# Kernel tuning notes

Hardware: AMD Instinct MI355X
Metric: run time of the kernel (lower is better)

## Reference

```python
import jax, jax.numpy as jnp
import numpy as np

E, K, D_IN, D_H, D_OUT, B = 16, 2, 256, 512, 256, 32768


def setup_inputs() -> dict:
    key = jax.random.key(0)
    ks = jax.random.split(key, 7)
    s_in = 1.0 / np.sqrt(D_IN)
    s_h = 1.0 / np.sqrt(D_H)
    return {
        "x": jax.random.normal(ks[0], (B, D_IN), jnp.float32),
        "Wg": jax.random.normal(ks[1], (D_IN, E), jnp.float32) * s_in,
        "bg": jnp.zeros((E,), jnp.float32),
        "W1": jax.random.normal(ks[2], (E, D_IN, D_H), jnp.float32) * s_in,
        "b1": jnp.zeros((E, D_H), jnp.float32),
        "W2": jax.random.normal(ks[3], (E, D_H, D_OUT), jnp.float32) * s_h,
        "b2": jnp.zeros((E, D_OUT), jnp.float32),
    }


def reference(x, Wg, bg, W1, b1, W2, b2):
    # Gating: softmax over experts, top-k, renormalize routing weights.
    probs = jax.nn.softmax(x @ Wg + bg, axis=-1)            # [B, E]
    top_vals, top_idx = jax.lax.top_k(probs, K)              # [B, K]
    w = top_vals / jnp.sum(top_vals, axis=-1, keepdims=True)  # [B, K]

    # Dense per-expert MLP over all tokens (vectorized dispatch equivalent).
    h = jax.nn.relu(jnp.einsum("bi,eih->ebh", x, W1) + b1[:, None, :])  # [E, B, Dh]
    out_e = jnp.einsum("ebh,eho->ebo", h, W2) + b2[:, None, :]          # [E, B, Do]

    # Gather each token's k assigned expert outputs and combine weighted.
    out_be = jnp.transpose(out_e, (1, 0, 2))                  # [B, E, Do]
    sel = jnp.take_along_axis(out_be, top_idx[:, :, None], axis=1)  # [B, K, Do]
    return jnp.sum(w[:, :, None] * sel, axis=1)               # [B, Do]
```

## Files before the change

### kernel.cpp

```cpp
#include <hip/hip_runtime.h>

#define E_ 16
#define DIN 256
#define DH 512
#define DOUT 256
#define BTOK 32768

typedef _Float16 half8 __attribute__((ext_vector_type(8)));
typedef _Float16 half4v __attribute__((ext_vector_type(4)));
typedef float float4v __attribute__((ext_vector_type(4)));

#define OFF_P1      0u
#define OFF_P2      4194304u
#define OFF_XH      8388608u
#define OFF_SCR     25165824u
#define OFF_TIDX    58720256u
#define OFF_TW      58982400u
#define OFF_STOK    59244544u
#define OFF_SW      59506688u
#define OFF_CNT     59768832u
#define OFF_OFFS    59768960u
#define OFF_CUR     59769088u
#define OFF_TMAP    59769216u
#define MLP_GRID    2048

__global__ __launch_bounds__(256) void pack_kernel(const float* __restrict__ W1,
                                                   const float* __restrict__ W2,
                                                   _Float16* __restrict__ p1,
                                                   _Float16* __restrict__ p2,
                                                   int* __restrict__ counts) {
    int tid = threadIdx.x;
    int bid = blockIdx.x * 4 + (tid >> 6);
    int l = tid & 63;
    int quad = l >> 4, l15 = l & 15;
    if (blockIdx.x == 0 && tid < 16) counts[tid] = 0;
    if (bid < 4096) {
        int ht = bid & 31, kt = (bid >> 5) & 7, e = bid >> 8;
        half8 v;
#pragma unroll
        for (int j = 0; j < 8; ++j)
            v[j] = (_Float16)W1[(e * DIN + kt * 32 + quad * 8 + j) * DH + ht * 16 + l15];
        ((half8*)p1)[bid * 64 + l] = v;
    } else {
        int b2i = bid - 4096;
        int ot = b2i & 15, kt = (b2i >> 4) & 15, e = b2i >> 8;
        half8 v;
#pragma unroll
        for (int j = 0; j < 8; ++j)
            v[j] = (_Float16)W2[(e * DH + kt * 32 + quad * 8 + j) * DOUT + ot * 16 + l15];
        ((half8*)p2)[b2i * 64 + l] = v;
    }
}

__global__ __launch_bounds__(256) void gate_kernel(const float* __restrict__ x,
                                                   const float* __restrict__ Wg,
                                                   const float* __restrict__ bg,
                                                   _Float16* __restrict__ xh,
                                                   int* __restrict__ tidx,
                                                   float* __restrict__ tw,
                                                   int* __restrict__ counts) {
    __shared__ float WgS[DIN * E_];
    __shared__ int hcnt[16];
    int tid = threadIdx.x;
    if (tid < 16) hcnt[tid] = 0;
#pragma unroll
    for (int i = 0; i < 4; ++i)
        ((float4v*)WgS)[tid + i * 256] = ((const float4v*)Wg)[tid + i * 256];
    __syncthreads();

    int q = tid & 7, tg = tid >> 3;
    int t0 = blockIdx.x * 64 + tg * 2;

    float acc[2][16];
#pragma unroll
    for (int tt = 0; tt < 2; ++tt)
#pragma unroll
        for (int e = 0; e < 16; ++e) acc[tt][e] = 0.f;

#pragma unroll
    for (int ii = 0; ii < 8; ++ii) {
        int kb = q * 32 + ii * 4;
        float4v xv[2];
#pragma unroll
        for (int tt = 0; tt < 2; ++tt) {
            xv[tt] = *(const float4v*)&x[(t0 + tt) * DIN + kb];
            half4v hv;
#pragma unroll
            for (int j = 0; j < 4; ++j) hv[j] = (_Float16)xv[tt][j];
            *(half4v*)&xh[(t0 + tt) * DIN + kb] = hv;
        }
#pragma unroll
        for (int j = 0; j < 4; ++j) {
            const float4v* wrow = (const float4v*)&WgS[(kb + j) * 16];
            float4v w0 = wrow[0], w1 = wrow[1], w2 = wrow[2], w3 = wrow[3];
#pragma unroll
            for (int tt = 0; tt < 2; ++tt) {
                float xs = xv[tt][j];
#pragma unroll
                for (int c = 0; c < 4; ++c) {
                    acc[tt][0 + c]  += xs * w0[c];
                    acc[tt][4 + c]  += xs * w1[c];
                    acc[tt][8 + c]  += xs * w2[c];
                    acc[tt][12 + c] += xs * w3[c];
                }
            }
        }
    }
#pragma unroll
    for (int tt = 0; tt < 2; ++tt)
#pragma unroll
        for (int e = 0; e < 16; ++e) {
            acc[tt][e] += __shfl_xor(acc[tt][e], 1);
            acc[tt][e] += __shfl_xor(acc[tt][e], 2);
            acc[tt][e] += __shfl_xor(acc[tt][e], 4);
        }
    if (q == 0) {
#pragma unroll
        for (int tt = 0; tt < 2; ++tt) {
            int b = t0 + tt;
            float m1 = -3.4e38f, m2 = -3.4e38f;
            int i1 = 0, i2 = 0;
#pragma unroll
            for (int e = 0; e < 16; ++e) {
                float v = acc[tt][e] + bg[e];
                if (v > m1) { m2 = m1; i2 = i1; m1 = v; i1 = e; }
                else if (v > m2) { m2 = v; i2 = e; }
            }
            float e2 = __expf(m2 - m1);
            float w1 = 1.f / (1.f + e2);
            tidx[b * 2] = i1; tidx[b * 2 + 1] = i2;
            tw[b * 2] = w1;  tw[b * 2 + 1] = e2 * w1;
            atomicAdd(&hcnt[i1], 1);
            atomicAdd(&hcnt[i2], 1);
        }
    }
    __syncthreads();
    if (tid < 16) atomicAdd(&counts[tid], hcnt[tid]);
}

__global__ void scan_kernel(const int* __restrict__ counts, int* __restrict__ offsets,
                            int* __restrict__ cursor, int* __restrict__ tmap) {
    __shared__ int s_off[17];
    int tid = threadIdx.x;
    for (int i = tid; i < MLP_GRID; i += 64) tmap[i] = -1;
    if (tid == 0) {
        int run = 0;
        for (int e = 0; e < 16; ++e) { s_off[e] = run; run += counts[e]; }
        s_off[16] = run;
    }
    __syncthreads();
    if (tid < 16) {
        int e = tid;
        offsets[e] = s_off[e];
        cursor[e] = s_off[e];
        if (e == 0) offsets[16] = s_off[16];
        int nt = (s_off[e + 1] - s_off[e] + 63) >> 6;
        int xc = e & 7;
        int base = (e >= 8) ? ((s_off[e - 7] - s_off[e - 8] + 63) >> 6) : 0;
        for (int t = 0; t < nt; ++t) {
            int s = base + t;
            if (s < 256) tmap[xc + 8 * s] = (e << 16) | t;
        }
    }
}

__global__ __launch_bounds__(256) void scatter_kernel(const int* __restrict__ tidx,
                                                      const float* __restrict__ tw,
                                                      int* __restrict__ cursor,
                                                      int* __restrict__ stok,
                                                      float* __restrict__ sw) {
    __shared__ int lc[16];
    __shared__ int lbase[16];
    int tid = threadIdx.x;
    if (tid < 16) lc[tid] = 0;
    __syncthreads();
    int g = blockIdx.x * 256 + tid;
    int e = tidx[g];
    int rank = atomicAdd(&lc[e], 1);
    __syncthreads();
    if (tid < 16) lbase[tid] = atomicAdd(&cursor[tid], lc[tid]);
    __syncthreads();
    int pos = lbase[e] + rank;
    stok[pos] = g;
    sw[pos] = tw[g];
}

#define XS 0
#define HS 16384
__global__ __launch_bounds__(512, 4) void mlp_kernel(const _Float16* __restrict__ xh,
                                                     const _Float16* __restrict__ p1,
                                                     const _Float16* __restrict__ p2,
                                                     const float* __restrict__ b1,
                                                     const float* __restrict__ b2,
                                                     const int* __restrict__ offsets,
                                                     const int* __restrict__ stok,
                                                     const float* __restrict__ sw,
                                                     const int* __restrict__ tmap,
                                                     _Float16* __restrict__ scr) {
    __shared__ _Float16 S[32768];
    const int tile = tmap[blockIdx.x];
    if (tile < 0) return;
    const int e = tile >> 16;
    const int ts = (tile & 0xffff) * 64;
    const int off = offsets[e];
    const int ne = offsets[e + 1] - off;
    const int rows = min(64, ne - ts);

    const int tid = threadIdx.x;
    const int w = tid >> 6;
    const int l = tid & 63;
    const int l15 = l & 15;
    const int quad = l >> 4;

#pragma unroll
    for (int j = 0; j < 4; ++j) {
        int tokl = w * 8 + j * 2 + (l >> 5);
        int slot = l & 31;
        int g = slot ^ (tokl & 7);
        int r = tokl; if (r >= rows) r = rows - 1;
        int tok = stok[off + ts + r] >> 1;
        half8 v = *(const half8*)&xh[tok * DIN + g * 8];
        *(half8*)&S[XS + tokl * 256 + slot * 8] = v;
    }

    const half8* p1b = (const half8*)p1;
    const half8* p2b = (const half8*)p2;

    float4v acc2[4][2];
#pragma unroll
    for (int mt = 0; mt < 4; ++mt)
#pragma unroll
        for (int n = 0; n < 2; ++n) acc2[mt][n] = (float4v){0.f, 0.f, 0.f, 0.f};

    __syncthreads();

#pragma unroll
    for (int half = 0; half < 2; ++half) {
        float4v acc1[2][4];
#pragma unroll
        for (int mh = 0; mh < 2; ++mh)
#pragma unroll
            for (int nt = 0; nt < 4; ++nt) acc1[mh][nt] = (float4v){0.f, 0.f, 0.f, 0.f};

#pragma unroll
        for (int kt = 0; kt < 8; ++kt) {
            half8 bq[4];
#pragma unroll
            for (int nt = 0; nt < 4; ++nt) {
                int row = nt * 16 + l15;
                int slot = (kt * 4 + quad) ^ (l15 & 7);
                bq[nt] = *(const half8*)&S[XS + row * 256 + slot * 8];
            }
#pragma unroll
            for (int mh = 0; mh < 2; ++mh) {
                half8 aw = p1b[((e * 8 + kt) * 32 + half * 16 + w * 2 + mh) * 64 + l];
#pragma unroll
                for (int nt = 0; nt < 4; ++nt)
                    acc1[mh][nt] = __builtin_amdgcn_mfma_f32_16x16x32_f16(aw, bq[nt], acc1[mh][nt], 0, 0, 0);
            }
        }
#pragma unroll
        for (int mh = 0; mh < 2; ++mh) {
            int colh = (w * 2 + mh) * 16 + quad * 4;
            float4v b1q = *(const float4v*)&b1[e * DH + half * 256 + colh];
            int gq = colh >> 3;
            int go = (quad & 1) * 4;
#pragma unroll
            for (int nt = 0; nt < 4; ++nt) {
                int row = nt * 16 + l15;
                int slot = gq ^ (l15 & 7);
                half4v hv;
#pragma unroll
                for (int r = 0; r < 4; ++r) {
                    float v = acc1[mh][nt][r] + b1q[r];
                    hv[r] = (_Float16)(v > 0.f ? v : 0.f);
                }
                *(half4v*)&S[HS + row * 256 + slot * 8 + go] = hv;
            }
        }
        __syncthreads();

#pragma unroll
        for (int kt2 = 0; kt2 < 8; ++kt2) {
            half8 ha[4];
#pragma unroll
            for (int mt = 0; mt < 4; ++mt) {
                int row = mt * 16 + l15;
                int slot = (kt2 * 4 + quad) ^ (l15 & 7);
                ha[mt] = *(const half8*)&S[HS + row * 256 + slot * 8];
            }
#pragma unroll
            for (int n = 0; n < 2; ++n) {
                half8 bw = p2b[((e * 16 + half * 8 + kt2) * 16 + w * 2 + n) * 64 + l];
#pragma unroll
                for (int mt = 0; mt < 4; ++mt)
                    acc2[mt][n] = __builtin_amdgcn_mfma_f32_16x16x32_f16(ha[mt], bw, acc2[mt][n], 0, 0, 0);
            }
        }
        __syncthreads();
    }

    float b2v[2];
#pragma unroll
    for (int n = 0; n < 2; ++n) b2v[n] = b2[e * DOUT + (w * 2 + n) * 16 + l15];
#pragma unroll
    for (int mt = 0; mt < 4; ++mt) {
#pragma unroll
        for (int r = 0; r < 4; ++r) {
            int row = mt * 16 + quad * 4 + r;
            int rc = row < rows ? row : rows - 1;
            float wt = sw[off + ts + rc];
#pragma unroll
            for (int n = 0; n < 2; ++n) {
                int col = (w * 2 + n) * 16 + l15;
                int slot = (col >> 3) ^ (row & 7);
                S[HS + row * 256 + slot * 8 + (col & 7)] =
                    (_Float16)(wt * (acc2[mt][n][r] + b2v[n]));
            }
        }
    }
    __syncthreads();
#pragma unroll
    for (int p = 0; p < 4; ++p) {
        int idx = p * 512 + tid;
        int tok = idx >> 5;
        int sl = idx & 31;
        if (tok < rows) {
            int slot = sl ^ (tok & 7);
            half8 v = *(const half8*)&S[HS + tok * 256 + slot * 8];
            int g = stok[off + ts + tok];
            *(half8*)&scr[g * DOUT + sl * 8] = v;
        }
    }
}

__global__ __launch_bounds__(256) void combine_kernel(const _Float16* __restrict__ scr,
                                                      float* __restrict__ out) {
    int wv = threadIdx.x >> 6;
    int l = threadIdx.x & 63;
    int t = blockIdx.x * 4 + wv;
    half4v a = ((const half4v*)(scr + t * 2 * DOUT))[l];
    half4v b = ((const half4v*)(scr + t * 2 * DOUT + DOUT))[l];
    float4v o;
#pragma unroll
    for (int j = 0; j < 4; ++j) o[j] = (float)a[j] + (float)b[j];
    ((float4v*)(out + t * DOUT))[l] = o;
}

extern "C" void kernel_launch(void* const* d_in, const int* in_sizes, int n_in,
                              void* d_out, int out_size, void* d_ws, size_t ws_size,
                              hipStream_t stream) {
    const float* x  = (const float*)d_in[0];
    const float* Wg = (const float*)d_in[1];
    const float* bg = (const float*)d_in[2];
    const float* W1 = (const float*)d_in[3];
    const float* b1 = (const float*)d_in[4];
    const float* W2 = (const float*)d_in[5];
    const float* b2 = (const float*)d_in[6];
    float* out = (float*)d_out;

    char* ws = (char*)d_ws;
    _Float16* p1  = (_Float16*)(ws + OFF_P1);
    _Float16* p2  = (_Float16*)(ws + OFF_P2);
    _Float16* xh  = (_Float16*)(ws + OFF_XH);
    _Float16* scr = (_Float16*)(ws + OFF_SCR);
    int* tidx     = (int*)(ws + OFF_TIDX);
    float* tw     = (float*)(ws + OFF_TW);
    int* stok     = (int*)(ws + OFF_STOK);
    float* swp    = (float*)(ws + OFF_SW);
    int* counts   = (int*)(ws + OFF_CNT);
    int* offsets  = (int*)(ws + OFF_OFFS);
    int* cursor   = (int*)(ws + OFF_CUR);
    int* tmap     = (int*)(ws + OFF_TMAP);

    pack_kernel<<<dim3(2048), dim3(256), 0, stream>>>(W1, W2, p1, p2, counts);
    gate_kernel<<<dim3(512), dim3(256), 0, stream>>>(x, Wg, bg, xh, tidx, tw, counts);
    scan_kernel<<<dim3(1), dim3(64), 0, stream>>>(counts, offsets, cursor, tmap);
    scatter_kernel<<<dim3(256), dim3(256), 0, stream>>>(tidx, tw, cursor, stok, swp);
    mlp_kernel<<<dim3(MLP_GRID), dim3(512), 0, stream>>>(xh, p1, p2, b1, b2, offsets,
                                                         stok, swp, tmap, scr);
    combine_kernel<<<dim3(8192), dim3(256), 0, stream>>>(scr, out);
}
```

Baseline: 220.7 us.

## Restructure gate kernel staging and drop MLP x-tile LDS staging

The gate kernel now stages 32 tokens of x in shared memory with coalesced loads and uses a padded Wg layout, with one token per 8 threads and twice as many blocks. The MLP kernel no longer copies token rows into shared memory. It reads the B fragments for the first GEMM straight from global xh, which halves LDS use and lets launch bounds ask for 8 blocks per CU. Weight loads use nontemporal hints, and the output epilogue packs pairs of halves through a lane shuffle to cut LDS store count. The trade-off is more global or L2 traffic from uncoalesced gathered xh reads in the inner loop, and higher register pressure under the tighter launch bound.

```diff
diff --git a/kernel.cpp b/kernel.cpp
--- a/kernel.cpp
+++ b/kernel.cpp
@@ -8,6 +8,7 @@
 
 typedef _Float16 half8 __attribute__((ext_vector_type(8)));
 typedef _Float16 half4v __attribute__((ext_vector_type(4)));
+typedef _Float16 half2v __attribute__((ext_vector_type(2)));
 typedef float float4v __attribute__((ext_vector_type(4)));
 
 #define OFF_P1      0u
@@ -59,80 +60,81 @@
                                                    int* __restrict__ tidx,
                                                    float* __restrict__ tw,
                                                    int* __restrict__ counts) {
-    __shared__ float WgS[DIN * E_];
+    __shared__ float XL[32 * 256];
+    __shared__ float WgS[256 * 17];
     __shared__ int hcnt[16];
-    int tid = threadIdx.x;
+    const int tid = threadIdx.x;
+    const int w = tid >> 6;
+    const int l = tid & 63;
     if (tid < 16) hcnt[tid] = 0;
-#pragma unroll
-    for (int i = 0; i < 4; ++i)
-        ((float4v*)WgS)[tid + i * 256] = ((const float4v*)Wg)[tid + i * 256];
-    __syncthreads();
-
-    int q = tid & 7, tg = tid >> 3;
-    int t0 = blockIdx.x * 64 + tg * 2;
-
-    float acc[2][16];
-#pragma unroll
-    for (int tt = 0; tt < 2; ++tt)
-#pragma unroll
-        for (int e = 0; e < 16; ++e) acc[tt][e] = 0.f;
+    {
+#pragma unroll
+        for (int j4 = 0; j4 < 4; ++j4) {
+            float4v v = *(const float4v*)&Wg[tid * 16 + j4 * 4];
+            WgS[tid * 17 + j4 * 4 + 0] = v[0];
+            WgS[tid * 17 + j4 * 4 + 1] = v[1];
+            WgS[tid * 17 + j4 * 4 + 2] = v[2];
+            WgS[tid * 17 + j4 * 4 + 3] = v[3];
+        }
+    }
+    const int t0 = blockIdx.x * 32;
+#pragma unroll
+    for (int i = 0; i < 8; ++i) {
+        int row = i * 4 + w;
+        float4v v = *(const float4v*)&x[(t0 + row) * DIN + l * 4];
+        *(float4v*)&XL[row * 256 + l * 4] = v;
+        half4v hv;
+#pragma unroll
+        for (int j = 0; j < 4; ++j) hv[j] = (_Float16)v[j];
+        *(half4v*)&xh[(t0 + row) * DIN + l * 4] = hv;
+    }
+    __syncthreads();
+
+    const int tok = tid >> 3, q = tid & 7;
+    float acc[16];
+#pragma unroll
+    for (int e = 0; e < 16; ++e) acc[e] = 0.f;
 
 #pragma unroll
     for (int ii = 0; ii < 8; ++ii) {
-        int kb = q * 32 + ii * 4;
-        float4v xv[2];
-#pragma unroll
-        for (int tt = 0; tt < 2; ++tt) {
-            xv[tt] = *(const float4v*)&x[(t0 + tt) * DIN + kb];
-            half4v hv;
-#pragma unroll
-            for (int j = 0; j < 4; ++j) hv[j] = (_Float16)xv[tt][j];
-            *(half4v*)&xh[(t0 + tt) * DIN + kb] = hv;
-        }
+        int kb = ii * 32 + q * 4;
+        float4v xv = *(const float4v*)&XL[tok * 256 + kb];
 #pragma unroll
         for (int j = 0; j < 4; ++j) {
-            const float4v* wrow = (const float4v*)&WgS[(kb + j) * 16];
-            float4v w0 = wrow[0], w1 = wrow[1], w2 = wrow[2], w3 = wrow[3];
-#pragma unroll
-            for (int tt = 0; tt < 2; ++tt) {
-                float xs = xv[tt][j];
-#pragma unroll
-                for (int c = 0; c < 4; ++c) {
-                    acc[tt][0 + c]  += xs * w0[c];
-                    acc[tt][4 + c]  += xs * w1[c];
-                    acc[tt][8 + c]  += xs * w2[c];
-                    acc[tt][12 + c] += xs * w3[c];
-                }
-            }
-        }
-    }
-#pragma unroll
-    for (int tt = 0; tt < 2; ++tt)
+            const float* wrow = &WgS[(kb + j) * 17];
+            float xs = xv[j];
+#pragma unroll
+            for (int e4 = 0; e4 < 4; ++e4) {
+                float4v w4 = *(const float4v*)&wrow[e4 * 4];
+                acc[e4 * 4 + 0] += xs * w4[0];
+                acc[e4 * 4 + 1] += xs * w4[1];
+                acc[e4 * 4 + 2] += xs * w4[2];
+                acc[e4 * 4 + 3] += xs * w4[3];
+            }
+        }
+    }
+#pragma unroll
+    for (int e = 0; e < 16; ++e) {
+        acc[e] += __shfl_xor(acc[e], 1);
+        acc[e] += __shfl_xor(acc[e], 2);
+        acc[e] += __shfl_xor(acc[e], 4);
+    }
+    if (q == 0) {
+        int b = t0 + tok;
+        float m1 = -3.4e38f, m2 = -3.4e38f;
+        int i1 = 0, i2 = 0;
 #pragma unroll
         for (int e = 0; e < 16; ++e) {
-            acc[tt][e] += __shfl_xor(acc[tt][e], 1);
-            acc[tt][e] += __shfl_xor(acc[tt][e], 2);
-            acc[tt][e] += __shfl_xor(acc[tt][e], 4);
-        }
-    if (q == 0) {
-#pragma unroll
-        for (int tt = 0; tt < 2; ++tt) {
-            int b = t0 + tt;
-            float m1 = -3.4e38f, m2 = -3.4e38f;
-            int i1 = 0, i2 = 0;
-#pragma unroll
-            for (int e = 0; e < 16; ++e) {
-                float v = acc[tt][e] + bg[e];
-                if (v > m1) { m2 = m1; i2 = i1; m1 = v; i1 = e; }
-                else if (v > m2) { m2 = v; i2 = e; }
-            }
-            float e2 = __expf(m2 - m1);
-            float w1 = 1.f / (1.f + e2);
-            tidx[b * 2] = i1; tidx[b * 2 + 1] = i2;
-            tw[b * 2] = w1;  tw[b * 2 + 1] = e2 * w1;
-            atomicAdd(&hcnt[i1], 1);
-            atomicAdd(&hcnt[i2], 1);
-        }
+            float v = acc[e] + bg[e];
+            if (v > m1) { m2 = m1; i2 = i1; m1 = v; i1 = e; }
+            else if (v > m2) { m2 = v; i2 = e; }
+        }
+        float e2 = __expf(m2 - m1);
+        float w1 = 1.f / (1.f + e2);
+        tidx[b * 2] = i1; tidx[b * 2 + 1] = i2;
+        tw[b * 2] = w1;  tw[b * 2 + 1] = e2 * w1;
+        atomicAdd(&hcnt[i1], 1);
+        atomicAdd(&hcnt[i2], 1);
     }
     __syncthreads();
     if (tid < 16) atomicAdd(&counts[tid], hcnt[tid]);
@@ -185,9 +187,7 @@
     sw[pos] = tw[g];
 }
 
-#define XS 0
-#define HS 16384
-__global__ __launch_bounds__(512, 4) void mlp_kernel(const _Float16* __restrict__ xh,
+__global__ __launch_bounds__(512, 8) void mlp_kernel(const _Float16* __restrict__ xh,
                                                      const _Float16* __restrict__ p1,
                                                      const _Float16* __restrict__ p2,
                                                      const float* __restrict__ b1,
@@ -197,7 +197,7 @@
                                                      const float* __restrict__ sw,
                                                      const int* __restrict__ tmap,
                                                      _Float16* __restrict__ scr) {
-    __shared__ _Float16 S[32768];
+    __shared__ _Float16 S[16384];
     const int tile = tmap[blockIdx.x];
     if (tile < 0) return;
     const int e = tile >> 16;
@@ -212,15 +212,11 @@
     const int l15 = l & 15;
     const int quad = l >> 4;
 
-#pragma unroll
-    for (int j = 0; j < 4; ++j) {
-        int tokl = w * 8 + j * 2 + (l >> 5);
-        int slot = l & 31;
-        int g = slot ^ (tokl & 7);
-        int r = tokl; if (r >= rows) r = rows - 1;
-        int tok = stok[off + ts + r] >> 1;
-        half8 v = *(const half8*)&xh[tok * DIN + g * 8];
-        *(half8*)&S[XS + tokl * 256 + slot * 8] = v;
+    const _Float16* tb[4];
+#pragma unroll
+    for (int nt = 0; nt < 4; ++nt) {
+        int r = nt * 16 + l15; if (r >= rows) r = rows - 1;
+        tb[nt] = xh + (stok[off + ts + r] >> 1) * DIN + quad * 8;
     }
 
     const half8* p1b = (const half8*)p1;
@@ -232,8 +228,6 @@
 #pragma unroll
         for (int n = 0; n < 2; ++n) acc2[mt][n] = (float4v){0.f, 0.f, 0.f, 0.f};
 
-    __syncthreads();
-
 #pragma unroll
     for (int half = 0; half < 2; ++half) {
         float4v acc1[2][4];
@@ -246,14 +240,11 @@
         for (int kt = 0; kt < 8; ++kt) {
             half8 bq[4];
 #pragma unroll
-            for (int nt = 0; nt < 4; ++nt) {
-                int row = nt * 16 + l15;
-                int slot = (kt * 4 + quad) ^ (l15 & 7);
-                bq[nt] = *(const half8*)&S[XS + row * 256 + slot * 8];
-            }
+            for (int nt = 0; nt < 4; ++nt) bq[nt] = *(const half8*)(tb[nt] + kt * 32);
 #pragma unroll
             for (int mh = 0; mh < 2; ++mh) {
-                half8 aw = p1b[((e * 8 + kt) * 32 + half * 16 + w * 2 + mh) * 64 + l];
+                half8 aw = __builtin_nontemporal_load(
+                    &p1b[((e * 8 + kt) * 32 + half * 16 + w * 2 + mh) * 64 + l]);
 #pragma unroll
                 for (int nt = 0; nt < 4; ++nt)
                     acc1[mh][nt] = __builtin_amdgcn_mfma_f32_16x16x32_f16(aw, bq[nt], acc1[mh][nt], 0, 0, 0);
@@ -275,7 +266,7 @@
                     float v = acc1[mh][nt][r] + b1q[r];
                     hv[r] = (_Float16)(v > 0.f ? v : 0.f);
                 }
-                *(half4v*)&S[HS + row * 256 + slot * 8 + go] = hv;
+                *(half4v*)&S[row * 256 + slot * 8 + go] = hv;
             }
         }
         __syncthreads();
@@ -287,11 +278,12 @@
             for (int mt = 0; mt < 4; ++mt) {
                 int row = mt * 16 + l15;
                 int slot = (kt2 * 4 + quad) ^ (l15 & 7);
-                ha[mt] = *(const half8*)&S[HS + row * 256 + slot * 8];
+                ha[mt] = *(const half8*)&S[row * 256 + slot * 8];
             }
 #pragma unroll
             for (int n = 0; n < 2; ++n) {
-                half8 bw = p2b[((e * 16 + half * 8 + kt2) * 16 + w * 2 + n) * 64 + l];
+                half8 bw = __builtin_nontemporal_load(
+                    &p2b[((e * 16 + half * 8 + kt2) * 16 + w * 2 + n) * 64 + l]);
 #pragma unroll
                 for (int mt = 0; mt < 4; ++mt)
                     acc2[mt][n] = __builtin_amdgcn_mfma_f32_16x16x32_f16(ha[mt], bw, acc2[mt][n], 0, 0, 0);
@@ -303,19 +295,35 @@
     float b2v[2];
 #pragma unroll
     for (int n = 0; n < 2; ++n) b2v[n] = b2[e * DOUT + (w * 2 + n) * 16 + l15];
+    const int even = (l15 & 1) == 0;
+    const int colp = (l15 & ~1);
 #pragma unroll
     for (int mt = 0; mt < 4; ++mt) {
+        float wt[4];
 #pragma unroll
         for (int r = 0; r < 4; ++r) {
             int row = mt * 16 + quad * 4 + r;
             int rc = row < rows ? row : rows - 1;
-            float wt = sw[off + ts + rc];
-#pragma unroll
-            for (int n = 0; n < 2; ++n) {
-                int col = (w * 2 + n) * 16 + l15;
-                int slot = (col >> 3) ^ (row & 7);
-                S[HS + row * 256 + slot * 8 + (col & 7)] =
-                    (_Float16)(wt * (acc2[mt][n][r] + b2v[n]));
+            wt[r] = sw[off + ts + rc];
+        }
+#pragma unroll
+        for (int n = 0; n < 2; ++n) {
+            float own[4], par[4];
+#pragma unroll
+            for (int r = 0; r < 4; ++r) {
+                own[r] = wt[r] * (acc2[mt][n][r] + b2v[n]);
+                par[r] = __shfl_xor(own[r], 1);
+            }
+            int cole = (w * 2 + n) * 16 + colp;
+#pragma unroll
+            for (int rr = 0; rr < 2; ++rr) {
+                int r = even ? rr : (2 + rr);
+                int row = mt * 16 + quad * 4 + r;
+                int slot = (cole >> 3) ^ (row & 7);
+                half2v hv;
+                hv[0] = (_Float16)(even ? own[r] : par[r]);
+                hv[1] = (_Float16)(even ? par[r] : own[r]);
+                *(half2v*)&S[row * 256 + slot * 8 + (cole & 7)] = hv;
             }
         }
     }
@@ -327,7 +335,7 @@
         int sl = idx & 31;
         if (tok < rows) {
             int slot = sl ^ (tok & 7);
-            half8 v = *(const half8*)&S[HS + tok * 256 + slot * 8];
+            half8 v = *(const half8*)&S[tok * 256 + slot * 8];
             int g = stok[off + ts + tok];
             *(half8*)&scr[g * DOUT + sl * 8] = v;
         }
@@ -374,7 +382,7 @@
     int* tmap     = (int*)(ws + OFF_TMAP);
 
     pack_kernel<<<dim3(2048), dim3(256), 0, stream>>>(W1, W2, p1, p2, counts);
-    gate_kernel<<<dim3(512), dim3(256), 0, stream>>>(x, Wg, bg, xh, tidx, tw, counts);
+    gate_kernel<<<dim3(1024), dim3(256), 0, stream>>>(x, Wg, bg, xh, tidx, tw, counts);
     scan_kernel<<<dim3(1), dim3(64), 0, stream>>>(counts, offsets, cursor, tmap);
     scatter_kernel<<<dim3(256), dim3(256), 0, stream>>>(tidx, tw, cursor, stok, swp);
     mlp_kernel<<<dim3(MLP_GRID), dim3(512), 0, stream>>>(xh, p1, p2, b1, b2, offsets,
```

Measured after the change: 484.9 us. 2.2x slower.
